# Kernel optimization log

Hardware: AMD Instinct MI355X
Metric: run time of the kernel (lower is better)

Reference implementation:

```python
import jax, jax.numpy as jnp
import numpy as np

B, LQ, LS, S = 64, 64, 512, 512
NEG = -1e6


def mask_for_lengths(lengths, max_len, mask_right=True):
    pos = jnp.arange(max_len)
    if mask_right:
        m = pos[None, :] >= lengths[:, None]
    else:
        m = pos[None, :] < lengths[:, None]
    return jnp.where(m, jnp.float32(NEG), jnp.float32(0.0))


def setup_inputs() -> dict:
    key = jax.random.key(0)
    ks = jax.random.split(key, 12)
    f = lambda k, shp: jax.random.normal(k, shp, jnp.float32)
    sc = np.float32(1.0 / np.sqrt(S))
    return {
        "encoded_question": f(ks[0], (B, LQ, S)),
        "encoded_support": f(ks[1], (B, LS, S)),
        "question_length": jax.random.randint(ks[2], (B,), 1, LQ + 1),
        "support_length": jax.random.randint(ks[3], (B,), LS // 2, LS + 1),
        "correct_start": jax.random.randint(ks[4], (B,), 0, LS),
        "answer2question": jnp.arange(B),
        "is_eval": 1,
        "W_qa": f(ks[5], (S, 1)) * sc,
        "W_qsi": f(ks[6], (S, S)) * sc,
        "b_qsi": jnp.zeros((S,), jnp.float32),
        "W_qs": f(ks[7], (2 * S, S)) * sc,
        "W_ss": f(ks[8], (S, 1)) * sc,
        "W_qei": f(ks[9], (S, S)) * sc,
        "b_qei": jnp.zeros((S,), jnp.float32),
        "W_qe": f(ks[10], (3 * S, S)) * sc,
        "W_es": f(ks[11], (S, 1)) * sc,
    }


def reference(encoded_question, encoded_support, question_length, support_length,
              correct_start, answer2question, is_eval,
              W_qa, W_qsi, b_qsi, W_qs, W_ss, W_qei, b_qei, W_qe, W_es):
    # question attention pooling
    att = jnp.einsum('bqd,do->bq', encoded_question, W_qa)
    att = att + mask_for_lengths(question_length, LQ)
    w = jax.nn.softmax(att, axis=1)                                   # [B,LQ]
    q_state = jnp.einsum('bqd,bq->bd', encoded_question, w)           # [B,S]

    # start scoring
    start_input = jnp.concatenate(
        [q_state[:, None, :] * encoded_support, encoded_support], axis=2)  # [B,LS,2S]
    q_start_inter = q_state @ W_qsi + b_qsi                           # [B,S]
    q_start_state = start_input @ W_qs + q_start_inter[:, None, :]    # [B,LS,S]
    support_mask = mask_for_lengths(support_length, LS)
    start_scores = jnp.einsum('bld,do->bl', jax.nn.relu(q_start_state), W_ss)
    start_scores = start_scores + support_mask                        # [B,LS]
    predicted_start_pointer = jnp.argmax(start_scores, axis=1)        # [B]

    # eval path: start_pointer = predicted argmax
    start_pointer = predicted_start_pointer
    u_s = jnp.take_along_axis(encoded_support,
                              start_pointer[:, None, None], axis=1)[:, 0, :]  # [B,S]

    # end scoring
    end_input = jnp.concatenate(
        [encoded_support * u_s[:, None, :], start_input], axis=2)     # [B,LS,3S]
    q_end_inter = q_state @ W_qei + b_qei
    q_end_state = end_input @ W_qe + q_end_inter[:, None, :]          # [B,LS,S]
    end_scores = jnp.einsum('bld,do->bl', jax.nn.relu(q_end_state), W_es)
    end_scores = end_scores + support_mask
    # eval: mask positions left of start_pointer
    end_scores = end_scores + mask_for_lengths(start_pointer, LS, mask_right=False)
    predicted_end_pointer = jnp.argmax(end_scores, axis=1)

    return (start_scores, end_scores, predicted_start_pointer, predicted_end_pointer)
```

## Files before the change

kernel.cpp:

```cpp
#include <hip/hip_runtime.h>
#include <math.h>

constexpr int B_  = 64;
constexpr int LQ_ = 64;
constexpr int LS_ = 512;
constexpr int S_  = 512;
#define NEGV (-1e6f)
#define MARGIN 0.0625f

typedef __attribute__((ext_vector_type(8))) short bf16x8;
typedef __attribute__((ext_vector_type(4))) float f32x4;

__device__ inline unsigned short f2bf_rn(float x) {
    unsigned u = __builtin_bit_cast(unsigned, x);
    unsigned r = (u + 0x7FFFu + ((u >> 16) & 1u)) >> 16;
    return (unsigned short)r;
}

__global__ __launch_bounds__(256)
void qpool_kernel(const float* __restrict__ eq, const int* __restrict__ qlen,
                  const float* __restrict__ W_qa, float* __restrict__ q_state)
{
    int b = blockIdx.x;
    int t = threadIdx.x;
    int wave = t >> 6, lane = t & 63;
    __shared__ float att[LQ_];
    __shared__ float wsm[LQ_];
    const float* eqb = eq + (size_t)b * LQ_ * S_;

    for (int k = 0; k < 16; ++k) {
        int q = wave + 4 * k;
        const float* row = eqb + q * S_;
        float s = 0.f;
        #pragma unroll
        for (int j = 0; j < S_ / 64; ++j)
            s = fmaf(row[lane + 64 * j], W_qa[lane + 64 * j], s);
        #pragma unroll
        for (int off = 32; off >= 1; off >>= 1)
            s += __shfl_xor(s, off);
        if (lane == 0) att[q] = s;
    }
    __syncthreads();

    if (wave == 0) {
        int L = qlen[b];
        float v = att[lane] + ((lane < L) ? 0.f : NEGV);
        float m = v;
        #pragma unroll
        for (int off = 32; off >= 1; off >>= 1)
            m = fmaxf(m, __shfl_xor(m, off));
        float e = expf(v - m);
        float sum = e;
        #pragma unroll
        for (int off = 32; off >= 1; off >>= 1)
            sum += __shfl_xor(sum, off);
        wsm[lane] = e / sum;
    }
    __syncthreads();

    for (int d = t; d < S_; d += 256) {
        float acc = 0.f;
        #pragma unroll 8
        for (int q = 0; q < LQ_; ++q)
            acc = fmaf(wsm[q], eqb[q * S_ + d], acc);
        q_state[b * S_ + d] = acc;
    }
}

__global__ __launch_bounds__(512)
void inter_kernel(const float* __restrict__ q_state,
                  const float* __restrict__ W_qsi, const float* __restrict__ b_qsi,
                  const float* __restrict__ W_qei, const float* __restrict__ b_qei,
                  float* __restrict__ qsi, float* __restrict__ qei)
{
    int b = blockIdx.x;
    const float* W  = blockIdx.y ? W_qei : W_qsi;
    const float* bi = blockIdx.y ? b_qei : b_qsi;
    float*       o  = blockIdx.y ? qei   : qsi;
    int t = threadIdx.x, lane = t & 63, w = t >> 6;
    __shared__ float qs[S_];
    __shared__ float red[8][S_];
    qs[t] = q_state[b * S_ + t];
    __syncthreads();

    float z[8];
    #pragma unroll
    for (int k = 0; k < 8; ++k) z[k] = 0.f;
    const int d0 = w * 64;
    #pragma unroll 4
    for (int dd = 0; dd < 64; ++dd) {
        int d = d0 + dd;
        float q = qs[d];
        const float* row = W + (size_t)d * S_ + lane;
        #pragma unroll
        for (int k = 0; k < 8; ++k)
            z[k] = fmaf(q, row[k * 64], z[k]);
    }
    #pragma unroll
    for (int k = 0; k < 8; ++k) red[w][k * 64 + lane] = z[k];
    __syncthreads();
    float acc = bi[t];
    #pragma unroll
    for (int ww = 0; ww < 8; ++ww) acc += red[ww][t];
    o[b * S_ + t] = acc;
}

template <int NT>
__global__ __launch_bounds__(512)
void prep_kernel(const float* __restrict__ W, const float* __restrict__ q_state,
                 const float* __restrict__ u_s, short* __restrict__ Wc)
{
    int bid = blockIdx.x;
    int i = bid >> 6, b = bid & 63;
    int col = threadIdx.x;
    __shared__ float scq[32], scu[32];
    if (col < 32) scq[col] = q_state[b * S_ + i * 32 + col];
    if (NT == 3 && col >= 32 && col < 64) scu[col - 32] = u_s[b * S_ + i * 32 + col - 32];
    __syncthreads();

    unsigned short h[32];
    #pragma unroll
    for (int d = 0; d < 32; ++d) {
        int D = i * 32 + d;
        float v;
        if (NT == 2)
            v = fmaf(scq[d], W[(size_t)D * S_ + col], W[(size_t)(S_ + D) * S_ + col]);
        else
            v = fmaf(scu[d], W[(size_t)D * S_ + col],
                fmaf(scq[d], W[(size_t)(S_ + D) * S_ + col], W[(size_t)(2 * S_ + D) * S_ + col]));
        h[d] = f2bf_rn(v);
    }
    size_t base = (size_t)b * 262144 + (size_t)i * 16384 + (size_t)col * 8;
    #pragma unroll
    for (int kc = 0; kc < 4; ++kc) {
        uint4 H;
        H.x = h[kc*8+0] | ((unsigned)h[kc*8+1] << 16);
        H.y = h[kc*8+2] | ((unsigned)h[kc*8+3] << 16);
        H.z = h[kc*8+4] | ((unsigned)h[kc*8+5] << 16);
        H.w = h[kc*8+6] | ((unsigned)h[kc*8+7] << 16);
        *(uint4*)&Wc[base + kc * 4096] = H;
    }
}

template <bool END>
__global__ __launch_bounds__(512, 4)
void score_kernel(const float* __restrict__ support, const short* __restrict__ Wc,
                  const float* __restrict__ inter, const float* __restrict__ Wsmall,
                  const int* __restrict__ slen, const int* __restrict__ sp,
                  float* __restrict__ out)
{
    const int t = threadIdx.x;
    const int lane = t & 63, wid = t >> 6;
    const int l15 = lane & 15, l4 = lane >> 4;

    int L = blockIdx.x;
    int xcd = L & 7, idx = L >> 3;
    int b = xcd * 8 + (idx & 7);
    int rc = idx >> 3;
    int l0 = rc * 64;

    __shared__ __attribute__((aligned(16))) short Bs[2][4][512][8];
    __shared__ __attribute__((aligned(16))) short As[2][4][64][8];
    __shared__ float int_l[S_], wsm_l[S_];
    __shared__ float sm_red[64][8];

    int_l[t] = inter[b * S_ + t];
    wsm_l[t] = Wsmall[t];

    const char* wc_bytes = (const char*)(Wc + (size_t)b * 262144);

    const int arow = t >> 3;
    const int akc  = (t >> 1) & 3;
    const int ahalf = t & 1;
    const float* supb = support + ((size_t)(b * LS_ + l0 + arow)) * S_ + akc * 8 + ahalf * 4;

    f32x4 acc[4][4];
    #pragma unroll
    for (int r = 0; r < 4; ++r)
        #pragma unroll
        for (int c = 0; c < 4; ++c)
            acc[r][c] = (f32x4){0.f, 0.f, 0.f, 0.f};

    auto stage = [&](int i, int pbuf) {
        const char* gb = wc_bytes + (size_t)i * 32768 + t * 16;
        char* lb = (char*)&Bs[pbuf][0][0][0] + t * 16;
        #pragma unroll
        for (int q = 0; q < 4; ++q)
            __builtin_amdgcn_global_load_lds(
                (const __attribute__((address_space(1))) void*)(gb + q * 8192),
                (__attribute__((address_space(3))) void*)(lb + q * 8192), 16, 0, 0);
    };
    auto buildA = [&](int pbuf, float4 v) {
        unsigned short h0 = f2bf_rn(v.x), h1 = f2bf_rn(v.y);
        unsigned short h2 = f2bf_rn(v.z), h3 = f2bf_rn(v.w);
        uint2 P;
        P.x = h0 | ((unsigned)h1 << 16);
        P.y = h2 | ((unsigned)h3 << 16);
        *(uint2*)&As[pbuf][akc][arow][ahalf * 4] = P;
    };

    float4 sv = *(const float4*)(supb);
    buildA(0, sv);
    stage(0, 0);
    float4 svn = *(const float4*)(supb + 32);

    for (int i = 0; i < 16; ++i) {
        const int par = i & 1;
        if (i + 1 < 16) {
            stage(i + 1, par ^ 1);
            buildA(par ^ 1, svn);
            if (i + 2 < 16) svn = *(const float4*)(supb + (i + 2) * 32);
            asm volatile("s_waitcnt vmcnt(5) lgkmcnt(0)" ::: "memory");
        } else {
            asm volatile("s_waitcnt vmcnt(0) lgkmcnt(0)" ::: "memory");
        }
        __builtin_amdgcn_s_barrier();

        bf16x8 ah[4];
        #pragma unroll
        for (int r = 0; r < 4; ++r)
            ah[r] = *(const bf16x8*)&As[par][l4][r * 16 + l15][0];
        #pragma unroll
        for (int c = 0; c < 4; ++c) {
            bf16x8 bh = *(const bf16x8*)&Bs[par][l4][wid * 64 + c * 16 + l15][0];
            #pragma unroll
            for (int r = 0; r < 4; ++r)
                acc[r][c] = __builtin_amdgcn_mfma_f32_16x16x32_bf16(ah[r], bh, acc[r][c], 0, 0, 0);
        }
        asm volatile("s_waitcnt lgkmcnt(0)" ::: "memory");
        __builtin_amdgcn_s_barrier();
    }

    #pragma unroll
    for (int r = 0; r < 4; ++r) {
        #pragma unroll
        for (int jj = 0; jj < 4; ++jj) {
            float pr = 0.f;
            #pragma unroll
            for (int c = 0; c < 4; ++c) {
                int col = wid * 64 + c * 16 + l15;
                float v = acc[r][c][jj] + int_l[col];
                v = fmaxf(v, 0.f);
                pr = fmaf(v, wsm_l[col], pr);
            }
            pr += __shfl_xor(pr, 1);
            pr += __shfl_xor(pr, 2);
            pr += __shfl_xor(pr, 4);
            pr += __shfl_xor(pr, 8);
            if (l15 == 0) sm_red[r * 16 + l4 * 4 + jj][wid] = pr;
        }
    }
    __syncthreads();
    if (t < 64) {
        int l = l0 + t;
        float s = 0.f;
        #pragma unroll
        for (int w = 0; w < 8; ++w) s += sm_red[t][w];
        if (l >= slen[b]) s += NEGV;
        if (END) { if (l < sp[b]) s += NEGV; }
        out[b * LS_ + l] = s;
    }
}

__device__ inline int select_cands(const float* s_l, int t, int lane, int w,
                                   float* wred, int* wcnt, int* cand)
{
    float v = s_l[t];
    #pragma unroll
    for (int off = 32; off >= 1; off >>= 1)
        v = fmaxf(v, __shfl_xor(v, off));
    if (lane == 0) wred[w] = v;
    __syncthreads();
    float m = wred[0];
    #pragma unroll
    for (int k = 1; k < 8; ++k) m = fmaxf(m, wred[k]);
    float th = m - MARGIN;
    bool flag = s_l[t] >= th;
    unsigned long long bal = __ballot(flag);
    int rank = __popcll(bal & ((1ull << lane) - 1ull));
    if (lane == 0) wcnt[w] = (int)__popcll(bal);
    __syncthreads();
    int off = 0, total = 0;
    #pragma unroll
    for (int k = 0; k < 8; ++k) { if (k < w) off += wcnt[k]; total += wcnt[k]; }
    if (flag) { int pos = off + rank; if (pos < 8) cand[pos] = t; }
    __syncthreads();
    return total < 8 ? total : 8;
}

template <bool END>
__global__ __launch_bounds__(512)
void rescue_kernel(const float* __restrict__ support, const float* __restrict__ q_state,
                   const float* __restrict__ u_s, const float* __restrict__ Wbig,
                   const float* __restrict__ inter, const float* __restrict__ Wsmall,
                   const float* __restrict__ scores, float* __restrict__ part)
{
    int bid = blockIdx.x;
    int b = bid >> 2, chunk = bid & 3;
    int t = threadIdx.x, lane = t & 63, w = t >> 6;
    __shared__ float s_l[S_], qs_l[S_], us_l[S_];
    __shared__ float arow[8][S_];
    __shared__ float red[8][8][128];
    __shared__ float wred[8];
    __shared__ int wcnt[8], cand[8];

    s_l[t]  = scores[b * S_ + t];
    qs_l[t] = q_state[b * S_ + t];
    if (END) us_l[t] = u_s[b * S_ + t];
    #pragma unroll
    for (int c = 0; c < 8; ++c) arow[c][t] = 0.f;
    __syncthreads();

    int cnt = select_cands(s_l, t, lane, w, wred, wcnt, cand);

    for (int c = 0; c < cnt; ++c)
        arow[c][t] = support[((size_t)(b * LS_ + cand[c])) * S_ + t];
    __syncthreads();

    float z0[8], z1[8];
    #pragma unroll
    for (int c = 0; c < 8; ++c) { z0[c] = 0.f; z1[c] = 0.f; }

    const int d0 = w * 64;
    const int s0 = chunk * 128 + lane, s1 = s0 + 64;
    const float* W1 = Wbig;
    const float* W2 = Wbig + (size_t)S_ * S_;
    const float* W3 = Wbig + (size_t)2 * S_ * S_;

    #pragma unroll 4
    for (int dd = 0; dd < 64; ++dd) {
        int d = d0 + dd;
        float r1a = W1[(size_t)d * S_ + s0], r1b = W1[(size_t)d * S_ + s1];
        float r2a = W2[(size_t)d * S_ + s0], r2b = W2[(size_t)d * S_ + s1];
        float r3a = 0.f, r3b = 0.f;
        if (END) { r3a = W3[(size_t)d * S_ + s0]; r3b = W3[(size_t)d * S_ + s1]; }
        float q = qs_l[d];
        float u = END ? us_l[d] : 0.f;
        #pragma unroll
        for (int c = 0; c < 8; ++c) {
            float a = arow[c][d];
            if (END) {
                float ua = u * a, qa = q * a;
                z0[c] = fmaf(ua, r1a, fmaf(qa, r2a, fmaf(a, r3a, z0[c])));
                z1[c] = fmaf(ua, r1b, fmaf(qa, r2b, fmaf(a, r3b, z1[c])));
            } else {
                float qa = q * a;
                z0[c] = fmaf(qa, r1a, fmaf(a, r2a, z0[c]));
                z1[c] = fmaf(qa, r1b, fmaf(a, r2b, z1[c]));
            }
        }
    }
    #pragma unroll
    for (int c = 0; c < 8; ++c) {
        red[w][c][lane]      = z0[c];
        red[w][c][64 + lane] = z1[c];
    }
    __syncthreads();

    {
        float a0 = 0.f, a1 = 0.f;
        #pragma unroll
        for (int ww = 0; ww < 8; ++ww) {
            a0 += red[ww][w][lane];
            a1 += red[ww][w][64 + lane];
        }
        float v0 = fmaxf(a0 + inter[b * S_ + s0], 0.f) * Wsmall[s0];
        float v1 = fmaxf(a1 + inter[b * S_ + s1], 0.f) * Wsmall[s1];
        float p = v0 + v1;
        #pragma unroll
        for (int off = 32; off >= 1; off >>= 1)
            p += __shfl_xor(p, off);
        if (lane == 0 && w < cnt) part[((size_t)b * 8 + w) * 4 + chunk] = p;
    }
}

template <bool END>
__global__ __launch_bounds__(512)
void finalize_kernel(const float* __restrict__ scores, const float* __restrict__ part,
                     const float* __restrict__ support, int* __restrict__ sp_ws,
                     float* __restrict__ pred, float* __restrict__ us_out)
{
    int b = blockIdx.x;
    int t = threadIdx.x, lane = t & 63, w = t >> 6;
    __shared__ float s_l[S_];
    __shared__ float wred[8];
    __shared__ int wcnt[8], cand[8];
    __shared__ int best_sh;

    s_l[t] = scores[b * S_ + t];
    __syncthreads();
    int cnt = select_cands(s_l, t, lane, w, wred, wcnt, cand);

    if (t == 0) {
        float bv = -INFINITY;
        int bi = cand[0];
        for (int c = 0; c < cnt; ++c) {
            const float* pp = part + ((size_t)b * 8 + c) * 4;
            float e = ((pp[0] + pp[1]) + pp[2]) + pp[3];
            if (e > bv) { bv = e; bi = cand[c]; }
        }
        best_sh = bi;
        pred[b] = (float)bi;
        if (!END) sp_ws[b] = bi;
    }
    __syncthreads();
    if (!END)
        us_out[b * S_ + t] = support[((size_t)(b * LS_ + best_sh)) * S_ + t];
}

extern "C" void kernel_launch(void* const* d_in, const int* in_sizes, int n_in,
                              void* d_out, int out_size, void* d_ws, size_t ws_size,
                              hipStream_t stream)
{
    const float* eq    = (const float*)d_in[0];
    const float* es    = (const float*)d_in[1];
    const int*   qlen  = (const int*)d_in[2];
    const int*   slen  = (const int*)d_in[3];
    const float* W_qa  = (const float*)d_in[7];
    const float* W_qsi = (const float*)d_in[8];
    const float* b_qsi = (const float*)d_in[9];
    const float* W_qs  = (const float*)d_in[10];
    const float* W_ss  = (const float*)d_in[11];
    const float* W_qei = (const float*)d_in[12];
    const float* b_qei = (const float*)d_in[13];
    const float* W_qe  = (const float*)d_in[14];
    const float* W_es  = (const float*)d_in[15];

    float* out          = (float*)d_out;
    float* start_scores = out;
    float* end_scores   = out + B_ * LS_;
    float* pred_start   = out + 2 * B_ * LS_;
    float* pred_end     = out + 2 * B_ * LS_ + B_;

    float* ws      = (float*)d_ws;
    float* q_state = ws;
    float* qsi     = ws + B_ * S_;
    float* qei     = ws + 2 * B_ * S_;
    float* u_s     = ws + 3 * B_ * S_;
    float* part    = ws + 4 * B_ * S_;
    int*   sp_ws   = (int*)(ws + 4 * B_ * S_ + 2048);
    short* Wc      = (short*)(ws + 4 * B_ * S_ + 2048 + 512);

    qpool_kernel<<<B_, 256, 0, stream>>>(eq, qlen, W_qa, q_state);
    inter_kernel<<<dim3(B_, 2), 512, 0, stream>>>(q_state, W_qsi, b_qsi, W_qei, b_qei, qsi, qei);

    prep_kernel<2><<<1024, 512, 0, stream>>>(W_qs, q_state, nullptr, Wc);
    score_kernel<false><<<512, 512, 0, stream>>>(es, Wc, qsi, W_ss, slen, nullptr, start_scores);
    rescue_kernel<false><<<256, 512, 0, stream>>>(es, q_state, nullptr, W_qs, qsi, W_ss,
                                                  start_scores, part);
    finalize_kernel<false><<<B_, 512, 0, stream>>>(start_scores, part, es, sp_ws, pred_start, u_s);

    prep_kernel<3><<<1024, 512, 0, stream>>>(W_qe, q_state, u_s, Wc);
    score_kernel<true><<<512, 512, 0, stream>>>(es, Wc, qei, W_es, slen, sp_ws, end_scores);
    rescue_kernel<true><<<256, 512, 0, stream>>>(es, q_state, u_s, W_qe, qei, W_es,
                                                 end_scores, part);
    finalize_kernel<true><<<B_, 512, 0, stream>>>(end_scores, part, es, nullptr, pred_end, nullptr);
}
```

Baseline: 169.6 us.

## Pre-convert support to bf16 once and retile score GEMM into 256x256 blocks

Adds a kernel that converts the support tensor to bf16 once in an MFMA-friendly layout, shared by both start and end scoring passes, replacing per-block on-the-fly fp32-to-bf16 conversion. The score kernel now computes 256x256 output tiles (split over rows and half the columns) with both A and B staged through global_load_lds, raising arithmetic intensity per loaded byte and cutting the B-matrix reloads of the prior 64-row tiles. Partial column-half sums are written to a scratch buffer and a new combine kernel adds them and applies the masks, adding two extra launches and extra global traffic. Occupancy drops to 2 blocks per CU and register use grows with the larger accumulator.

Result: slower. 190.4 us (+12.3%).

```diff
diff --git a/kernel.cpp b/kernel.cpp
--- a/kernel.cpp
+++ b/kernel.cpp
@@ -15,6 +15,38 @@
     unsigned u = __builtin_bit_cast(unsigned, x);
     unsigned r = (u + 0x7FFFu + ((u >> 16) & 1u)) >> 16;
     return (unsigned short)r;
+}
+
+__global__ __launch_bounds__(512)
+void prep_support_kernel(const float* __restrict__ support, short* __restrict__ Aprep)
+{
+    int bid = blockIdx.x;
+    int b = bid >> 3, rg = bid & 7;
+    int t = threadIdx.x;
+    int r  = t & 63;
+    int cg = t >> 6;
+    int row  = rg * 64 + r;
+    int rc   = row >> 8;
+    int rowp = row & 255;
+    const float* src = support + ((size_t)(b * LS_ + row)) * S_;
+
+    #pragma unroll
+    for (int ii = 0; ii < 2; ++ii) {
+        int i = cg * 2 + ii;
+        #pragma unroll
+        for (int kc = 0; kc < 4; ++kc) {
+            int d0 = i * 32 + kc * 8;
+            float4 f0 = *(const float4*)(src + d0);
+            float4 f1 = *(const float4*)(src + d0 + 4);
+            uint4 H;
+            H.x = f2bf_rn(f0.x) | ((unsigned)f2bf_rn(f0.y) << 16);
+            H.y = f2bf_rn(f0.z) | ((unsigned)f2bf_rn(f0.w) << 16);
+            H.z = f2bf_rn(f1.x) | ((unsigned)f2bf_rn(f1.y) << 16);
+            H.w = f2bf_rn(f1.z) | ((unsigned)f2bf_rn(f1.w) << 16);
+            size_t off = ((size_t)(b * 2 + rc) * 16 + i) * 8192 + kc * 2048 + rowp * 8;
+            *(uint4*)&Aprep[off] = H;
+        }
+    }
 }
 
 __global__ __launch_bounds__(256)
@@ -113,6 +145,7 @@
     int bid = blockIdx.x;
     int i = bid >> 6, b = bid & 63;
     int col = threadIdx.x;
+    int cc = col >> 8, colp = col & 255;
     __shared__ float scq[32], scu[32];
     if (col < 32) scq[col] = q_state[b * S_ + i * 32 + col];
     if (NT == 3 && col >= 32 && col < 64) scu[col - 32] = u_s[b * S_ + i * 32 + col - 32];
@@ -130,7 +163,7 @@
                 fmaf(scq[d], W[(size_t)(S_ + D) * S_ + col], W[(size_t)(2 * S_ + D) * S_ + col]));
         h[d] = f2bf_rn(v);
     }
-    size_t base = (size_t)b * 262144 + (size_t)i * 16384 + (size_t)col * 8;
+    size_t base = ((size_t)(b * 2 + cc) * 16 + i) * 8192 + (size_t)colp * 8;
     #pragma unroll
     for (int kc = 0; kc < 4; ++kc) {
         uint4 H;
@@ -138,93 +171,89 @@
         H.y = h[kc*8+2] | ((unsigned)h[kc*8+3] << 16);
         H.z = h[kc*8+4] | ((unsigned)h[kc*8+5] << 16);
         H.w = h[kc*8+6] | ((unsigned)h[kc*8+7] << 16);
-        *(uint4*)&Wc[base + kc * 4096] = H;
-    }
-}
-
-template <bool END>
-__global__ __launch_bounds__(512, 4)
-void score_kernel(const float* __restrict__ support, const short* __restrict__ Wc,
+        *(uint4*)&Wc[base + kc * 2048] = H;
+    }
+}
+
+__global__ __launch_bounds__(512, 2)
+void score_kernel(const short* __restrict__ Aprep, const short* __restrict__ Wc,
                   const float* __restrict__ inter, const float* __restrict__ Wsmall,
-                  const int* __restrict__ slen, const int* __restrict__ sp,
                   float* __restrict__ out)
 {
     const int t = threadIdx.x;
     const int lane = t & 63, wid = t >> 6;
+    const int wr = wid >> 2, wc = wid & 3;
     const int l15 = lane & 15, l4 = lane >> 4;
 
-    int L = blockIdx.x;
-    int xcd = L & 7, idx = L >> 3;
-    int b = xcd * 8 + (idx & 7);
-    int rc = idx >> 3;
-    int l0 = rc * 64;
-
-    __shared__ __attribute__((aligned(16))) short Bs[2][4][512][8];
-    __shared__ __attribute__((aligned(16))) short As[2][4][64][8];
-    __shared__ float int_l[S_], wsm_l[S_];
-    __shared__ float sm_red[64][8];
-
-    int_l[t] = inter[b * S_ + t];
-    wsm_l[t] = Wsmall[t];
-
-    const char* wc_bytes = (const char*)(Wc + (size_t)b * 262144);
-
-    const int arow = t >> 3;
-    const int akc  = (t >> 1) & 3;
-    const int ahalf = t & 1;
-    const float* supb = support + ((size_t)(b * LS_ + l0 + arow)) * S_ + akc * 8 + ahalf * 4;
-
-    f32x4 acc[4][4];
-    #pragma unroll
-    for (int r = 0; r < 4; ++r)
+    int lid = blockIdx.x;
+    int xcd = lid & 7, slot = lid >> 3;
+    int b  = xcd * 8 + (slot >> 2);
+    int rc = (slot >> 1) & 1;
+    int cc = slot & 1;
+
+    __shared__ __attribute__((aligned(16))) short As[2][8192];
+    __shared__ __attribute__((aligned(16))) short Bs[2][8192];
+    __shared__ float int_l[256], wsm_l[256];
+    __shared__ float sm_red[256][4];
+
+    if (t < 256) {
+        int_l[t] = inter[b * S_ + cc * 256 + t];
+        wsm_l[t] = Wsmall[cc * 256 + t];
+    }
+
+    const char* Abase = (const char*)(Aprep + ((size_t)(b * 2 + rc) * 16) * 8192);
+    const char* Bbase = (const char*)(Wc    + ((size_t)(b * 2 + cc) * 16) * 8192);
+
+    f32x4 acc[8][4];
+    #pragma unroll
+    for (int r = 0; r < 8; ++r)
         #pragma unroll
         for (int c = 0; c < 4; ++c)
             acc[r][c] = (f32x4){0.f, 0.f, 0.f, 0.f};
 
-    auto stage = [&](int i, int pbuf) {
-        const char* gb = wc_bytes + (size_t)i * 32768 + t * 16;
-        char* lb = (char*)&Bs[pbuf][0][0][0] + t * 16;
-        #pragma unroll
-        for (int q = 0; q < 4; ++q)
-            __builtin_amdgcn_global_load_lds(
-                (const __attribute__((address_space(1))) void*)(gb + q * 8192),
-                (__attribute__((address_space(3))) void*)(lb + q * 8192), 16, 0, 0);
+    auto stage = [&](int i, int buf) {
+        const char* ga = Abase + (size_t)i * 16384 + t * 16;
+        const char* gb = Bbase + (size_t)i * 16384 + t * 16;
+        char* la = (char*)As[buf] + t * 16;
+        char* lb = (char*)Bs[buf] + t * 16;
+        __builtin_amdgcn_global_load_lds(
+            (const __attribute__((address_space(1))) void*)ga,
+            (__attribute__((address_space(3))) void*)la, 16, 0, 0);
+        __builtin_amdgcn_global_load_lds(
+            (const __attribute__((address_space(1))) void*)(ga + 8192),
+            (__attribute__((address_space(3))) void*)(la + 8192), 16, 0, 0);
+        __builtin_amdgcn_global_load_lds(
+            (const __attribute__((address_space(1))) void*)gb,
+            (__attribute__((address_space(3))) void*)lb, 16, 0, 0);
+        __builtin_amdgcn_global_load_lds(
+            (const __attribute__((address_space(1))) void*)(gb + 8192),
+            (__attribute__((address_space(3))) void*)(lb + 8192), 16, 0, 0);
     };
-    auto buildA = [&](int pbuf, float4 v) {
-        unsigned short h0 = f2bf_rn(v.x), h1 = f2bf_rn(v.y);
-        unsigned short h2 = f2bf_rn(v.z), h3 = f2bf_rn(v.w);
-        uint2 P;
-        P.x = h0 | ((unsigned)h1 << 16);
-        P.y = h2 | ((unsigned)h3 << 16);
-        *(uint2*)&As[pbuf][akc][arow][ahalf * 4] = P;
-    };
-
-    float4 sv = *(const float4*)(supb);
-    buildA(0, sv);
+
     stage(0, 0);
-    float4 svn = *(const float4*)(supb + 32);
 
     for (int i = 0; i < 16; ++i) {
-        const int par = i & 1;
+        const int buf = i & 1;
         if (i + 1 < 16) {
-            stage(i + 1, par ^ 1);
-            buildA(par ^ 1, svn);
-            if (i + 2 < 16) svn = *(const float4*)(supb + (i + 2) * 32);
-            asm volatile("s_waitcnt vmcnt(5) lgkmcnt(0)" ::: "memory");
+            stage(i + 1, buf ^ 1);
+            asm volatile("s_waitcnt vmcnt(4)" ::: "memory");
         } else {
-            asm volatile("s_waitcnt vmcnt(0) lgkmcnt(0)" ::: "memory");
+            asm volatile("s_waitcnt vmcnt(0)" ::: "memory");
         }
         __builtin_amdgcn_s_barrier();
 
-        bf16x8 ah[4];
-        #pragma unroll
-        for (int r = 0; r < 4; ++r)
-            ah[r] = *(const bf16x8*)&As[par][l4][r * 16 + l15][0];
+        bf16x8 ah[8];
+        #pragma unroll
+        for (int r = 0; r < 8; ++r) {
+            int rowp = wr * 128 + r * 16 + l15;
+            ah[r] = *(const bf16x8*)&As[buf][l4 * 2048 + rowp * 8];
+        }
         #pragma unroll
         for (int c = 0; c < 4; ++c) {
-            bf16x8 bh = *(const bf16x8*)&Bs[par][l4][wid * 64 + c * 16 + l15][0];
+            int colp = wc * 64 + c * 16 + l15;
+            bf16x8 bh = *(const bf16x8*)&Bs[buf][l4 * 2048 + colp * 8];
             #pragma unroll
-            for (int r = 0; r < 4; ++r)
+            for (int r = 0; r < 8; ++r)
                 acc[r][c] = __builtin_amdgcn_mfma_f32_16x16x32_bf16(ah[r], bh, acc[r][c], 0, 0, 0);
         }
         asm volatile("s_waitcnt lgkmcnt(0)" ::: "memory");
@@ -232,34 +261,43 @@
     }
 
     #pragma unroll
-    for (int r = 0; r < 4; ++r) {
+    for (int r = 0; r < 8; ++r) {
         #pragma unroll
         for (int jj = 0; jj < 4; ++jj) {
             float pr = 0.f;
             #pragma unroll
             for (int c = 0; c < 4; ++c) {
-                int col = wid * 64 + c * 16 + l15;
-                float v = acc[r][c][jj] + int_l[col];
+                int colp = wc * 64 + c * 16 + l15;
+                float v = acc[r][c][jj] + int_l[colp];
                 v = fmaxf(v, 0.f);
-                pr = fmaf(v, wsm_l[col], pr);
+                pr = fmaf(v, wsm_l[colp], pr);
             }
             pr += __shfl_xor(pr, 1);
             pr += __shfl_xor(pr, 2);
             pr += __shfl_xor(pr, 4);
             pr += __shfl_xor(pr, 8);
-            if (l15 == 0) sm_red[r * 16 + l4 * 4 + jj][wid] = pr;
-        }
-    }
-    __syncthreads();
-    if (t < 64) {
-        int l = l0 + t;
-        float s = 0.f;
-        #pragma unroll
-        for (int w = 0; w < 8; ++w) s += sm_red[t][w];
-        if (l >= slen[b]) s += NEGV;
-        if (END) { if (l < sp[b]) s += NEGV; }
-        out[b * LS_ + l] = s;
-    }
+            if (l15 == 0) sm_red[wr * 128 + r * 16 + l4 * 4 + jj][wc] = pr;
+        }
+    }
+    __syncthreads();
+    if (t < 256) {
+        int l = rc * 256 + t;
+        float s = sm_red[t][0] + sm_red[t][1] + sm_red[t][2] + sm_red[t][3];
+        out[((size_t)cc * B_ * LS_) + b * LS_ + l] = s;
+    }
+}
+
+__global__ __launch_bounds__(256)
+void combine_kernel(const float* __restrict__ part0, const float* __restrict__ part1,
+                    const int* __restrict__ slen, const int* __restrict__ sp,
+                    int endflag, float* __restrict__ out)
+{
+    int g = blockIdx.x * 256 + threadIdx.x;
+    int b = g >> 9, l = g & 511;
+    float s = part0[g] + part1[g];
+    if (l >= slen[b]) s += NEGV;
+    if (endflag && l < sp[b]) s += NEGV;
+    out[g] = s;
 }
 
 __device__ inline int select_cands(const float* s_l, int t, int lane, int w,
@@ -439,19 +477,26 @@
     float* u_s     = ws + 3 * B_ * S_;
     float* part    = ws + 4 * B_ * S_;
     int*   sp_ws   = (int*)(ws + 4 * B_ * S_ + 2048);
-    short* Wc      = (short*)(ws + 4 * B_ * S_ + 2048 + 512);
-
+    float* scpart  = ws + 4 * B_ * S_ + 4096;
+    short* Wc      = (short*)(scpart + 2 * B_ * LS_);
+    short* Aprep   = Wc + (size_t)B_ * 2 * 16 * 8192;
+
+    prep_support_kernel<<<512, 512, 0, stream>>>(es, Aprep);
     qpool_kernel<<<B_, 256, 0, stream>>>(eq, qlen, W_qa, q_state);
     inter_kernel<<<dim3(B_, 2), 512, 0, stream>>>(q_state, W_qsi, b_qsi, W_qei, b_qei, qsi, qei);
 
     prep_kernel<2><<<1024, 512, 0, stream>>>(W_qs, q_state, nullptr, Wc);
-    score_kernel<false><<<512, 512, 0, stream>>>(es, Wc, qsi, W_ss, slen, nullptr, start_scores);
+    score_kernel<<<256, 512, 0, stream>>>(Aprep, Wc, qsi, W_ss, scpart);
+    combine_kernel<<<B_ * LS_ / 256, 256, 0, stream>>>(scpart, scpart + B_ * LS_,
+                                                       slen, sp_ws, 0, start_scores);
     rescue_kernel<false><<<256, 512, 0, stream>>>(es, q_state, nullptr, W_qs, qsi, W_ss,
                                                   start_scores, part);
     finalize_kernel<false><<<B_, 512, 0, stream>>>(start_scores, part, es, sp_ws, pred_start, u_s);
 
     prep_kernel<3><<<1024, 512, 0, stream>>>(W_qe, q_state, u_s, Wc);
-    score_kernel<true><<<512, 512, 0, stream>>>(es, Wc, qei, W_es, slen, sp_ws, end_scores);
+    score_kernel<<<256, 512, 0, stream>>>(Aprep, Wc, qei, W_es, scpart);
+    combine_kernel<<<B_ * LS_ / 256, 256, 0, stream>>>(scpart, scpart + B_ * LS_,
+                                                       slen, sp_ws, 1, end_scores);
     rescue_kernel<true><<<256, 512, 0, stream>>>(es, q_state, u_s, W_qe, qei, W_es,
                                                  end_scores, part);
     finalize_kernel<true><<<B_, 512, 0, stream>>>(end_scores, part, es, nullptr, pred_end, nullptr);
```
